# Optimization experiments

Measured on AMD Instinct MI355X. Metric: run time of the kernel, lower is better.

Reference implementation:

```python
import jax, jax.numpy as jnp
import numpy as np

N = 8192       # nodes
IN_F = 512     # in_features
OUT_F = 256    # out_features


def setup_inputs() -> dict:
    key = jax.random.key(0)
    k1, k2, k3, k4 = jax.random.split(key, 4)
    # xavier_uniform-like scales for params
    w_scale = 1.414 * (6.0 / (IN_F + OUT_F)) ** 0.5
    a_scale = 1.414 * (6.0 / (2 * OUT_F + 1)) ** 0.5
    x = jax.random.normal(k1, (N, IN_F), jnp.float32)
    W = jax.random.uniform(k2, (IN_F, OUT_F), jnp.float32, -w_scale, w_scale)
    a = jax.random.uniform(k3, (2 * OUT_F, 1), jnp.float32, -a_scale, a_scale)
    adj = jax.random.randint(k4, (N, N), 0, 2, jnp.int32)
    return {"x": x, "W": W, "a": a, "adj": adj}


def reference(x, W, a, adj):
    # h = x @ W : [N, OUT_F]
    h = x @ W
    f = W.shape[1]
    a1, a2 = a[:f], a[f:]          # each [OUT_F, 1]
    # Original builds a_input[i,j] = concat(h_i, h_j) then matmuls with a.
    # Equivalent decomposition: e[i,j] = h_i . a1 + h_j . a2
    e = (h @ a1) + (h @ a2).T      # [N, N]
    neg = jnp.float32(-9e15)
    attention = jnp.where(adj > 0, e, neg)   # no softmax in the original
    h_prime = attention @ h        # [N, OUT_F]
    return h_prime
```

## Files before the change

### kernel.cpp

```cpp
#include <hip/hip_runtime.h>


#define NEG_BIG (-9000000000000000.0f)
#define POS_BIG (9000000000000000.0f)

typedef __bf16 bf16x8 __attribute__((ext_vector_type(8)));
typedef float f32x16 __attribute__((ext_vector_type(16)));

static __device__ __forceinline__ unsigned short f2bf(float f) {
  unsigned u = __builtin_bit_cast(unsigned, f);
  u = u + 0x7FFFu + ((u >> 16) & 1u);
  return (unsigned short)(u >> 16);
}
static __device__ __forceinline__ float bfbits2f(unsigned hi16) {
  return __builtin_bit_cast(float, hi16 << 16);
}
static __device__ __forceinline__ unsigned pk2(float a, float b) {
  return (unsigned)f2bf(a) | ((unsigned)f2bf(b) << 16);
}
static __device__ __forceinline__ unsigned m2(int a, int b) {
  return (unsigned)(a + (b << 16)) * 0x3F80u;
}
static __device__ __forceinline__ bf16x8 asbf(int4 q) {
  return __builtin_bit_cast(bf16x8, q);
}
static __device__ __forceinline__ f32x16 mfma(bf16x8 a, int4 b, f32x16 c) {
  return __builtin_amdgcn_mfma_f32_32x32x16_bf16(a, asbf(b), c, 0, 0, 0);
}

__global__ void k1a_wt(const float* __restrict__ W, unsigned short* __restrict__ WT,
                       float* __restrict__ T) {
  const int i = blockIdx.x * 256 + threadIdx.x;
  const int k = i >> 8, n = i & 255;
  WT[n * 512 + k] = f2bf(W[i]);
  if (blockIdx.x == 0) T[threadIdx.x] = 0.f;
}

__global__ __launch_bounds__(256) void k1b_h(const float* __restrict__ x,
    const unsigned short* __restrict__ WT, unsigned short* __restrict__ hP) {
  const int t = threadIdx.x;
  const int w = t >> 6, l = t & 63, l31 = l & 31, lh = l >> 5;
  const int gw = blockIdx.x * 4 + w;
  const int mt = gw >> 3, nt = gw & 7;
  const int m0 = mt << 5, n0 = nt << 5;
  f32x16 acc;
  for (int i = 0; i < 16; ++i) acc[i] = 0.f;
  const float* xr = x + (size_t)(m0 + l31) * 512 + lh * 8;
  const unsigned short* wr = WT + (size_t)(n0 + l31) * 512 + lh * 8;
#pragma unroll 4
  for (int k0 = 0; k0 < 512; k0 += 16) {
    float4 xa = *(const float4*)(xr + k0);
    float4 xb = *(const float4*)(xr + k0 + 4);
    int4 wb = *(const int4*)(wr + k0);
    union { unsigned u[4]; bf16x8 v; } A;
    A.u[0] = pk2(xa.x, xa.y); A.u[1] = pk2(xa.z, xa.w);
    A.u[2] = pk2(xb.x, xb.y); A.u[3] = pk2(xb.z, xb.w);
    acc = __builtin_amdgcn_mfma_f32_32x32x16_bf16(A.v, asbf(wb), acc, 0, 0, 0);
  }
#pragma unroll
  for (int reg = 0; reg < 16; ++reg) {
    const int m = m0 + (reg & 3) + 8 * (reg >> 2) + 4 * lh;
    const int n = n0 + l31;
    hP[(size_t)(m >> 5) * 8192 + n * 32 + (m & 31)] = f2bf(acc[reg]);
  }
}

__global__ __launch_bounds__(256) void k2_colsum(const unsigned short* __restrict__ hP,
                                                 float* __restrict__ T) {
  const int t = threadIdx.x;
  const int b = blockIdx.x;
  const int4* p = (const int4*)(hP + (size_t)b * 8192 + t * 32);
  int4 q0 = p[0], q1 = p[1], q2 = p[2], q3 = p[3];
  float s = 0.f;
  const unsigned* u0 = (const unsigned*)&q0;
  const unsigned* u1 = (const unsigned*)&q1;
  const unsigned* u2 = (const unsigned*)&q2;
  const unsigned* u3 = (const unsigned*)&q3;
#pragma unroll
  for (int i = 0; i < 4; ++i) {
    s += bfbits2f(u0[i] & 0xFFFFu) + bfbits2f(u0[i] >> 16);
    s += bfbits2f(u1[i] & 0xFFFFu) + bfbits2f(u1[i] >> 16);
    s += bfbits2f(u2[i] & 0xFFFFu) + bfbits2f(u2[i] >> 16);
    s += bfbits2f(u3[i] & 0xFFFFu) + bfbits2f(u3[i] >> 16);
  }
  atomicAdd(&T[t], s);
}

__global__ void k2b_init(const float* __restrict__ T, float* __restrict__ out) {
  const int i = blockIdx.x * 256 + threadIdx.x;
  const int n4 = (i & 63) * 4;
  float4 tv = *(const float4*)(T + n4);
  float4 o;
  o.x = NEG_BIG * tv.x; o.y = NEG_BIG * tv.y;
  o.z = NEG_BIG * tv.z; o.w = NEG_BIG * tv.w;
  ((float4*)out)[i] = o;
}

#define A_LSTR 68
template<int MODE>
__global__ __launch_bounds__(256, 2) void k3_att(const int* __restrict__ adj,
    const unsigned short* __restrict__ hP, float* __restrict__ outp) {
  __shared__ unsigned short S[4][2][32 * A_LSTR];
  const int t = threadIdx.x;
  const int blk = blockIdx.x;
  const int s = blk & 7;
  const int g = blk >> 3;
  const int w = t >> 6;
  const int rtile = g * 4 + w;
  const int l = t & 63;
  const int l31 = l & 31, lh = l >> 5;
  const int R0 = rtile * 32;

  const int sr = l >> 4;
  const int sc = (l & 15) << 2;
  const int* aB = adj + (size_t)(R0 + sr) * 8192 + s * 1024 + sc;
  unsigned short* const S0 = &S[w][0][0];
  unsigned short* const S1 = &S[w][1][0];
  const int woff = sr * A_LSTR + sc;

  f32x16 acc[8];
#pragma unroll
  for (int nt = 0; nt < 8; ++nt)
#pragma unroll
    for (int i = 0; i < 16; ++i) acc[nt][i] = 0.f;

#define LOADS(dst, it)                                                     \
  _Pragma("unroll")                                                        \
  for (int q = 0; q < 8; ++q)                                              \
    dst[q] = *(const int4*)(aB + (size_t)q * 4 * 8192 + (it) * 64);
#define PACKW(buf, src)                                                    \
  _Pragma("unroll")                                                        \
  for (int q = 0; q < 8; ++q)                                              \
    *(uint2*)(buf + woff + q * 4 * A_LSTR) =                               \
        make_uint2(m2(src[q].x, src[q].y), m2(src[q].z, src[q].w));

  int4 gA[8], gB[8];
  LOADS(gA, 0)
  LOADS(gB, 1)
  PACKW(S0, gA)

  const unsigned short* hW = hP + (size_t)s * 32 * 8192 + (size_t)l31 * 32 + lh * 8;

#define COMPUTE(it, buf)                                                   \
  {                                                                        \
    const unsigned short* hB = hW + (size_t)(it) * 2 * 8192;               \
    _Pragma("unroll")                                                      \
    for (int ks = 0; ks < 4; ++ks) {                                       \
      const bf16x8 Af =                                                    \
          *(const bf16x8*)(buf + l31 * A_LSTR + ks * 16 + lh * 8);         \
      const unsigned short* hk = hB + (ks >> 1) * 8192 + (ks & 1) * 16;    \
      _Pragma("unroll")                                                    \
      for (int nt = 0; nt < 8; ++nt) {                                     \
        int4 bq = *(const int4*)(hk + nt * 1024);                          \
        acc[nt] = mfma(Af, bq, acc[nt]);                                   \
      }                                                                    \
    }                                                                      \
  }

#pragma unroll 1
  for (int it = 0; it < 16; it += 2) {
    if (it + 2 < 16) { LOADS(gA, it + 2) }
    PACKW(S1, gB)
    COMPUTE(it, S0)
    if (it + 3 < 16) { LOADS(gB, it + 3) }
    if (it + 2 < 16) { PACKW(S0, gA) }
    COMPUTE(it + 1, S1)
  }

#pragma unroll
  for (int nt = 0; nt < 8; ++nt) {
    const int nn = nt * 32 + l31;
#pragma unroll
    for (int reg = 0; reg < 16; ++reg) {
      const int rr = R0 + (reg & 3) + 8 * (reg >> 2) + 4 * lh;
      if (MODE == 0) {
        outp[(size_t)s * 2097152 + (size_t)rr * 256 + nn] = acc[nt][reg];
      } else {
        atomicAdd(outp + (size_t)rr * 256 + nn, POS_BIG * acc[nt][reg]);
      }
    }
  }
}

__global__ __launch_bounds__(256) void k4_reduce(const float* __restrict__ P,
    const float* __restrict__ T, float* __restrict__ out) {
  const int i = blockIdx.x * 256 + threadIdx.x;
  float4 tv = *(const float4*)(T + (i & 63) * 4);
  const float4* P4 = (const float4*)P;
  float sx = 0.f, sy = 0.f, sz = 0.f, sw = 0.f;
#pragma unroll
  for (int sp = 0; sp < 8; ++sp) {
    float4 v = P4[(size_t)sp * 524288 + i];
    sx += v.x; sy += v.y; sz += v.z; sw += v.w;
  }
  float4 o;
  o.x = POS_BIG * sx + NEG_BIG * tv.x;
  o.y = POS_BIG * sy + NEG_BIG * tv.y;
  o.z = POS_BIG * sz + NEG_BIG * tv.z;
  o.w = POS_BIG * sw + NEG_BIG * tv.w;
  ((float4*)out)[i] = o;
}

extern "C" void kernel_launch(void* const* d_in, const int* in_sizes, int n_in,
                              void* d_out, int out_size, void* d_ws, size_t ws_size,
                              hipStream_t stream) {
  const float* x = (const float*)d_in[0];
  const float* W = (const float*)d_in[1];
  const int* adj = (const int*)d_in[3];
  float* out = (float*)d_out;
  char* ws = (char*)d_ws;
  unsigned short* WT = (unsigned short*)(ws);
  unsigned short* hP = (unsigned short*)(ws + (1 << 20));
  float* T = (float*)(ws + (6 << 20));
  float* P = (float*)(ws + (8 << 20));

  const bool fit = ws_size >= ((size_t)(8 << 20) + (size_t)64 * 1024 * 1024);

  k1a_wt<<<512, 256, 0, stream>>>(W, WT, T);
  k1b_h<<<512, 256, 0, stream>>>(x, WT, hP);
  k2_colsum<<<256, 256, 0, stream>>>(hP, T);
  if (fit) {
    k3_att<0><<<512, 256, 0, stream>>>(adj, hP, P);
    k4_reduce<<<2048, 256, 0, stream>>>(P, T, out);
  } else {
    k2b_init<<<2048, 256, 0, stream>>>(T, out);
    k3_att<1><<<512, 256, 0, stream>>>(adj, hP, out);
  }
}
```

Before: 485.8 us.

## Split attention output columns across wave pairs and stage x in LDS for h GEMM

The attention kernel now gives each wave half of the 256 output columns instead of all of them. That halves the accumulator registers per wave and doubles the grid, and the hP operands are prefetched into registers before each MFMA batch through a new LDS layout for the adjacency mask. The cost is that both waves in a pair load and pack the same adjacency rows, doubling adjacency reads. The h projection kernel converts each 32-row slice of x to bf16 once in shared memory, and each wave computes two output tiles from it, removing redundant x loads and conversions.

```diff
diff --git a/kernel.cpp b/kernel.cpp
--- a/kernel.cpp
+++ b/kernel.cpp
@@ -38,30 +38,40 @@
 
 __global__ __launch_bounds__(256) void k1b_h(const float* __restrict__ x,
     const unsigned short* __restrict__ WT, unsigned short* __restrict__ hP) {
+  __shared__ unsigned short XS[64 * 264];
   const int t = threadIdx.x;
+  const int mt = blockIdx.x;
+  const int m0 = mt << 5;
+  const int row = t >> 3, c7 = t & 7;
+  const float* xr = x + (size_t)(m0 + row) * 512 + c7 * 4;
+  const int gb = c7 >> 1, off = (t & 1) * 4;
+#pragma unroll
+  for (int j = 0; j < 16; ++j) {
+    float4 v = *(const float4*)(xr + 32 * j);
+    *(uint2*)&XS[(gb + 4 * j) * 264 + row * 8 + off] =
+        make_uint2(pk2(v.x, v.y), pk2(v.z, v.w));
+  }
+  __syncthreads();
   const int w = t >> 6, l = t & 63, l31 = l & 31, lh = l >> 5;
-  const int gw = blockIdx.x * 4 + w;
-  const int mt = gw >> 3, nt = gw & 7;
-  const int m0 = mt << 5, n0 = nt << 5;
-  f32x16 acc;
-  for (int i = 0; i < 16; ++i) acc[i] = 0.f;
-  const float* xr = x + (size_t)(m0 + l31) * 512 + lh * 8;
-  const unsigned short* wr = WT + (size_t)(n0 + l31) * 512 + lh * 8;
+  f32x16 acc0, acc1;
+  for (int i = 0; i < 16; ++i) { acc0[i] = 0.f; acc1[i] = 0.f; }
+  const int nt0 = w * 2;
+  const unsigned short* w0 = WT + (size_t)(nt0 * 32 + l31) * 512 + lh * 8;
+  const unsigned short* w1 = w0 + 32 * 512;
+  const char* XB = (const char*)XS + lh * 528 + l31 * 16;
 #pragma unroll 4
-  for (int k0 = 0; k0 < 512; k0 += 16) {
-    float4 xa = *(const float4*)(xr + k0);
-    float4 xb = *(const float4*)(xr + k0 + 4);
-    int4 wb = *(const int4*)(wr + k0);
-    union { unsigned u[4]; bf16x8 v; } A;
-    A.u[0] = pk2(xa.x, xa.y); A.u[1] = pk2(xa.z, xa.w);
-    A.u[2] = pk2(xb.x, xb.y); A.u[3] = pk2(xb.z, xb.w);
-    acc = __builtin_amdgcn_mfma_f32_32x32x16_bf16(A.v, asbf(wb), acc, 0, 0, 0);
+  for (int ks = 0; ks < 32; ++ks) {
+    bf16x8 Af = *(const bf16x8*)(XB + ks * 1056);
+    int4 b0 = *(const int4*)(w0 + ks * 16);
+    int4 b1 = *(const int4*)(w1 + ks * 16);
+    acc0 = mfma(Af, b0, acc0);
+    acc1 = mfma(Af, b1, acc1);
   }
 #pragma unroll
   for (int reg = 0; reg < 16; ++reg) {
-    const int m = m0 + (reg & 3) + 8 * (reg >> 2) + 4 * lh;
-    const int n = n0 + l31;
-    hP[(size_t)(m >> 5) * 8192 + n * 32 + (m & 31)] = f2bf(acc[reg]);
+    const int mm = (reg & 3) + 8 * (reg >> 2) + 4 * lh;
+    hP[(size_t)mt * 8192 + (nt0 * 32 + l31) * 32 + mm] = f2bf(acc0[reg]);
+    hP[(size_t)mt * 8192 + ((nt0 + 1) * 32 + l31) * 32 + mm] = f2bf(acc1[reg]);
   }
 }
 
@@ -96,83 +106,92 @@
   ((float4*)out)[i] = o;
 }
 
-#define A_LSTR 68
 template<int MODE>
 __global__ __launch_bounds__(256, 2) void k3_att(const int* __restrict__ adj,
     const unsigned short* __restrict__ hP, float* __restrict__ outp) {
-  __shared__ unsigned short S[4][2][32 * A_LSTR];
-  const int t = threadIdx.x;
-  const int blk = blockIdx.x;
+  __shared__ unsigned short S[4][2][8 * 264];
+  const int t = threadIdx.x, blk = blockIdx.x;
   const int s = blk & 7;
-  const int g = blk >> 3;
-  const int w = t >> 6;
-  const int rtile = g * 4 + w;
-  const int l = t & 63;
-  const int l31 = l & 31, lh = l >> 5;
-  const int R0 = rtile * 32;
-
-  const int sr = l >> 4;
-  const int sc = (l & 15) << 2;
-  const int* aB = adj + (size_t)(R0 + sr) * 8192 + s * 1024 + sc;
-  unsigned short* const S0 = &S[w][0][0];
-  unsigned short* const S1 = &S[w][1][0];
-  const int woff = sr * A_LSTR + sc;
-
-  f32x16 acc[8];
-#pragma unroll
-  for (int nt = 0; nt < 8; ++nt)
+  const int rg = blk >> 3;
+  const int w = t >> 6, l = t & 63, l31 = l & 31, lh = l >> 5;
+  const int rtile = rg * 2 + (w >> 1);
+  const int nh = w & 1;
+  const int sr = l >> 4, j4 = (l & 15) << 2;
+  const int* aB = adj + (size_t)(rtile * 32 + sr) * 8192 + s * 1024 + j4;
+  unsigned short* const Sw0 = &S[w][0][0];
+  unsigned short* const Sw1 = &S[w][1][0];
+  const int woff = (j4 >> 3) * 264 + sr * 8 + (j4 & 7);
+
+  const unsigned short* hB = hP + (size_t)(s * 32) * 8192
+                              + (size_t)(nh * 128 + l31) * 32 + lh * 8;
+
+  f32x16 acc[4];
+#pragma unroll
+  for (int nt = 0; nt < 4; ++nt)
 #pragma unroll
     for (int i = 0; i < 16; ++i) acc[nt][i] = 0.f;
 
-#define LOADS(dst, it)                                                     \
-  _Pragma("unroll")                                                        \
-  for (int q = 0; q < 8; ++q)                                              \
+  int4 gA[8], gB[8], Bv[16];
+
+#define ALOAD(dst, it)                                                      \
+  _Pragma("unroll")                                                         \
+  for (int q = 0; q < 8; ++q)                                               \
     dst[q] = *(const int4*)(aB + (size_t)q * 4 * 8192 + (it) * 64);
-#define PACKW(buf, src)                                                    \
-  _Pragma("unroll")                                                        \
-  for (int q = 0; q < 8; ++q)                                              \
-    *(uint2*)(buf + woff + q * 4 * A_LSTR) =                               \
+#define APACK(buf, src)                                                     \
+  _Pragma("unroll")                                                         \
+  for (int q = 0; q < 8; ++q)                                               \
+    *(uint2*)&buf[woff + q * 32] =                                          \
         make_uint2(m2(src[q].x, src[q].y), m2(src[q].z, src[q].w));
-
-  int4 gA[8], gB[8];
-  LOADS(gA, 0)
-  LOADS(gB, 1)
-  PACKW(S0, gA)
-
-  const unsigned short* hW = hP + (size_t)s * 32 * 8192 + (size_t)l31 * 32 + lh * 8;
-
-#define COMPUTE(it, buf)                                                   \
-  {                                                                        \
-    const unsigned short* hB = hW + (size_t)(it) * 2 * 8192;               \
-    _Pragma("unroll")                                                      \
-    for (int ks = 0; ks < 4; ++ks) {                                       \
-      const bf16x8 Af =                                                    \
-          *(const bf16x8*)(buf + l31 * A_LSTR + ks * 16 + lh * 8);         \
-      const unsigned short* hk = hB + (ks >> 1) * 8192 + (ks & 1) * 16;    \
-      _Pragma("unroll")                                                    \
-      for (int nt = 0; nt < 8; ++nt) {                                     \
-        int4 bq = *(const int4*)(hk + nt * 1024);                          \
-        acc[nt] = mfma(Af, bq, acc[nt]);                                   \
-      }                                                                    \
-    }                                                                      \
-  }
+#define BLOAD(it)                                                           \
+  {                                                                         \
+    const unsigned short* hb = hB + (size_t)(it) * 2 * 8192;                \
+    _Pragma("unroll")                                                       \
+    for (int pb = 0; pb < 2; ++pb)                                          \
+      _Pragma("unroll")                                                     \
+      for (int kh = 0; kh < 2; ++kh)                                        \
+        _Pragma("unroll")                                                   \
+        for (int nt = 0; nt < 4; ++nt)                                      \
+          Bv[(pb * 2 + kh) * 4 + nt] =                                      \
+              *(const int4*)(hb + pb * 8192 + nt * 1024 + kh * 16);         \
+  }
+#define COMP(buf)                                                           \
+  {                                                                         \
+    const char* Ab = (const char*)(buf) + lh * 528 + l31 * 16;              \
+    _Pragma("unroll")                                                       \
+    for (int ks = 0; ks < 4; ++ks) {                                        \
+      bf16x8 Af = *(const bf16x8*)(Ab + ks * 1056);                         \
+      _Pragma("unroll")                                                     \
+      for (int nt = 0; nt < 4; ++nt)                                        \
+        acc[nt] = mfma(Af, Bv[ks * 4 + nt], acc[nt]);                       \
+    }                                                                       \
+  }
+
+  ALOAD(gA, 0)
+  ALOAD(gB, 1)
+  APACK(Sw0, gA)
 
 #pragma unroll 1
-  for (int it = 0; it < 16; it += 2) {
-    if (it + 2 < 16) { LOADS(gA, it + 2) }
-    PACKW(S1, gB)
-    COMPUTE(it, S0)
-    if (it + 3 < 16) { LOADS(gB, it + 3) }
-    if (it + 2 < 16) { PACKW(S0, gA) }
-    COMPUTE(it + 1, S1)
-  }
-
-#pragma unroll
-  for (int nt = 0; nt < 8; ++nt) {
-    const int nn = nt * 32 + l31;
+  for (int r = 0; r < 16; r += 2) {
+    BLOAD(r)
+    if (r + 2 < 16) { ALOAD(gA, r + 2) }
+    APACK(Sw1, gB)
+    COMP(Sw0)
+    BLOAD(r + 1)
+    if (r + 3 < 16) { ALOAD(gB, r + 3) }
+    if (r + 2 < 16) { APACK(Sw0, gA) }
+    COMP(Sw1)
+  }
+#undef ALOAD
+#undef APACK
+#undef BLOAD
+#undef COMP
+
+#pragma unroll
+  for (int nt = 0; nt < 4; ++nt) {
+    const int nn = nh * 128 + nt * 32 + l31;
 #pragma unroll
     for (int reg = 0; reg < 16; ++reg) {
-      const int rr = R0 + (reg & 3) + 8 * (reg >> 2) + 4 * lh;
+      const int rr = rtile * 32 + (reg & 3) + 8 * (reg >> 2) + 4 * lh;
       if (MODE == 0) {
         outp[(size_t)s * 2097152 + (size_t)rr * 256 + nn] = acc[nt][reg];
       } else {
@@ -217,13 +236,13 @@
   const bool fit = ws_size >= ((size_t)(8 << 20) + (size_t)64 * 1024 * 1024);
 
   k1a_wt<<<512, 256, 0, stream>>>(W, WT, T);
-  k1b_h<<<512, 256, 0, stream>>>(x, WT, hP);
+  k1b_h<<<256, 256, 0, stream>>>(x, WT, hP);
   k2_colsum<<<256, 256, 0, stream>>>(hP, T);
   if (fit) {
-    k3_att<0><<<512, 256, 0, stream>>>(adj, hP, P);
+    k3_att<0><<<1024, 256, 0, stream>>>(adj, hP, P);
     k4_reduce<<<2048, 256, 0, stream>>>(P, T, out);
   } else {
     k2b_init<<<2048, 256, 0, stream>>>(T, out);
-    k3_att<1><<<512, 256, 0, stream>>>(adj, hP, out);
-  }
-}
+    k3_att<1><<<1024, 256, 0, stream>>>(adj, hP, out);
+  }
+}
```

Measured after the change: 473.0 us. 2.6% less time.
